# Kernel optimization log

Measured on AMD Instinct MI355X. Metric: run time of the kernel, lower is better.

The kernel has to match this reference:

```python
import jax, jax.numpy as jnp
import numpy as np

CHUNK_SIZE = 64
EPS = 1e-6


def setup_inputs() -> dict:
    key = jax.random.key(0)
    ks = jax.random.split(key, 5)
    B, NH, S, DH = 2, 16, 4096, 64
    return {
        "q": jax.random.normal(ks[0], (B, NH, S, DH), dtype=jnp.float32),
        "k": jax.random.normal(ks[1], (B, NH, S, DH), dtype=jnp.float32),
        "v": jax.random.normal(ks[2], (B, NH, S, DH), dtype=jnp.float32),
        "igate_preact": jax.random.normal(ks[3], (B, NH, S), dtype=jnp.float32),
        "fgate_preact": jax.random.normal(ks[4], (B, NH, S), dtype=jnp.float32),
    }


def _mlstm_intra(q, k, v, ig, fg, chunk_size, eps):
    # q,k,v: [B,NH,S,DH]; ig,fg: [B,NH,S]
    B, NH, S, DH = q.shape
    L = chunk_size
    NC = S // L
    qc = q.reshape(B, NH, NC, L, DH)
    kc = k.reshape(B, NH, NC, L, DH)
    vc = v.reshape(B, NH, NC, L, DH)
    igc = ig.reshape(B, NH, NC, L)
    fgc = fg.reshape(B, NH, NC, L)

    # log forget gates and their within-chunk cumulative sums
    log_fg = jax.nn.log_sigmoid(fgc)                      # [B,NH,NC,L]
    log_fg_cum = jnp.cumsum(log_fg, axis=-1)              # [B,NH,NC,L]

    # gated decay matrix: logD[i,j] = sum_{t=j+1..i} log f_t + i_j  for j<=i
    log_fg_mat = log_fg_cum[..., :, None] - log_fg_cum[..., None, :]  # [B,NH,NC,L,L]
    log_D = log_fg_mat + igc[..., None, :]
    causal = jnp.tril(jnp.ones((L, L), dtype=bool))
    log_D = jnp.where(causal, log_D, -jnp.inf)

    # stabilizer (row-wise max)
    m = jnp.max(log_D, axis=-1)                           # [B,NH,NC,L]
    D = jnp.exp(log_D - m[..., None])                     # [B,NH,NC,L,L]

    # QK scores scaled, gated by decay matrix
    scale = 1.0 / jnp.sqrt(jnp.asarray(DH, dtype=q.dtype))
    scores = jnp.einsum("bncld,bncsd->bncls", qc, kc) * scale
    C = scores * D                                        # [B,NH,NC,L,L]

    # stabilized normalizer: max(|row sum|, exp(-m))
    n = jnp.maximum(jnp.abs(jnp.sum(C, axis=-1)), jnp.exp(-m))  # [B,NH,NC,L]
    h = jnp.einsum("bncls,bncsd->bncld", C, vc) / (n[..., None] + eps)
    return h.reshape(B, NH, S, DH)


def reference(q, k, v, igate_preact, fgate_preact):
    return _mlstm_intra(q, k, v, igate_preact, fgate_preact, CHUNK_SIZE, EPS)
```

## Files before the change

kernel.cpp:

```cpp
#include <hip/hip_runtime.h>
#include <hip/hip_bf16.h>
#include <math.h>

namespace {

typedef __bf16 bf16x8 __attribute__((ext_vector_type(8)));
typedef float f32x4 __attribute__((ext_vector_type(4)));

constexpr int L = 64;
constexpr int DH = 64;

__device__ __forceinline__ int kkey(int r) { return (r ^ (r >> 2)) & 7; }
__device__ __forceinline__ int swzV(int d, int j) {
  return d * 128 + ((((j >> 3) ^ kkey(d)) & 7) << 4) + (j & 7) * 2;
}
__device__ __forceinline__ int swzC(int r, int j) {
  return r * 128 + ((((j >> 3) ^ kkey(r)) & 7) << 4) + (j & 7) * 2;
}

__device__ __forceinline__ unsigned short bfbits(float f) {
  __bf16 h = (__bf16)f;
  return __builtin_bit_cast(unsigned short, h);
}
__device__ __forceinline__ __bf16 tobf(float f) { return (__bf16)f; }

__global__ __launch_bounds__(64, 2) void mlstm_mfma(
    const float* __restrict__ q, const float* __restrict__ k,
    const float* __restrict__ v, const float* __restrict__ ig,
    const float* __restrict__ fg, float* __restrict__ out) {

  __shared__ __align__(16) char vt_raw[64 * 128];
  __shared__ __align__(16) char cs_raw[64 * 128];
  __shared__ __align__(16) float ea_sh[64];
  __shared__ float eb_sh[64], em_sh[64];

  const int lane = threadIdx.x;
  const int m = lane & 15;
  const int g = lane >> 4;
  const size_t cbase = (size_t)blockIdx.x * (L * DH);
  const size_t gb = (size_t)blockIdx.x * L;

  const float fgv = fg[gb + lane];
  const float igv = ig[gb + lane];

  const float4* v4 = (const float4*)(v + cbase);
  float4 vbuf[16];
#pragma unroll
  for (int it = 0; it < 16; ++it) vbuf[it] = v4[it * 64 + lane];

  float4 qbuf[4][2][2], kbuf[4][2][2];
#pragma unroll
  for (int rb = 0; rb < 4; ++rb)
#pragma unroll
    for (int kb = 0; kb < 2; ++kb) {
      const int off = (rb * 16 + m) * 64 + kb * 32 + g * 8;
      qbuf[rb][kb][0] = *(const float4*)(q + cbase + off);
      qbuf[rb][kb][1] = *(const float4*)(q + cbase + off + 4);
      kbuf[rb][kb][0] = *(const float4*)(k + cbase + off);
      kbuf[rb][kb][1] = *(const float4*)(k + cbase + off + 4);
    }

  {
    const float lf = fminf(fgv, 0.f) - log1pf(__expf(-fabsf(fgv)));
    float cum = lf;
#pragma unroll
    for (int o = 1; o < 64; o <<= 1) {
      const float t = __shfl_up(cum, o, 64);
      if (lane >= o) cum += t;
    }
    const float a = igv - cum;
    float b = a;
#pragma unroll
    for (int o = 1; o < 64; o <<= 1) {
      const float t = __shfl_up(b, o, 64);
      if (lane >= o) b = fmaxf(b, t);
    }
    const float bmax = __shfl(b, 63, 64);
    ea_sh[lane] = 0.125f * __expf(a - bmax);
    eb_sh[lane] = __expf(bmax - b);
    em_sh[lane] = __expf(-(b + cum));
  }

  {
    unsigned short* vt = (unsigned short*)vt_raw;
#pragma unroll
    for (int it = 0; it < 16; ++it) {
      const int idx = it * 64 + lane;
      const int j = idx >> 4;
      const int d0 = (idx & 15) * 4;
      vt[swzV(d0 + 0, j) >> 1] = bfbits(vbuf[it].x);
      vt[swzV(d0 + 1, j) >> 1] = bfbits(vbuf[it].y);
      vt[swzV(d0 + 2, j) >> 1] = bfbits(vbuf[it].z);
      vt[swzV(d0 + 3, j) >> 1] = bfbits(vbuf[it].w);
    }
  }

  bf16x8 qf[4][2], kf[4][2];
#pragma unroll
  for (int rb = 0; rb < 4; ++rb)
#pragma unroll
    for (int kb = 0; kb < 2; ++kb) {
      const float4 q0 = qbuf[rb][kb][0], q1 = qbuf[rb][kb][1];
      const float4 k0 = kbuf[rb][kb][0], k1 = kbuf[rb][kb][1];
      qf[rb][kb] = bf16x8{tobf(q0.x), tobf(q0.y), tobf(q0.z), tobf(q0.w),
                          tobf(q1.x), tobf(q1.y), tobf(q1.z), tobf(q1.w)};
      kf[rb][kb] = bf16x8{tobf(k0.x), tobf(k0.y), tobf(k0.z), tobf(k0.w),
                          tobf(k1.x), tobf(k1.y), tobf(k1.z), tobf(k1.w)};
    }

  f32x4 st[4][4];
#pragma unroll
  for (int cb = 0; cb < 4; ++cb)
#pragma unroll
    for (int rb = 0; rb < 4; ++rb) {
      if (rb > cb) continue;
      f32x4 acc = {0.f, 0.f, 0.f, 0.f};
      acc = __builtin_amdgcn_mfma_f32_16x16x32_bf16(kf[rb][0], qf[cb][0], acc, 0, 0, 0);
      acc = __builtin_amdgcn_mfma_f32_16x16x32_bf16(kf[rb][1], qf[cb][1], acc, 0, 0, 0);
      st[rb][cb] = acc;
    }

  bf16x8 vfr[4][2];
#pragma unroll
  for (int db = 0; db < 4; ++db)
#pragma unroll
    for (int jb = 0; jb < 2; ++jb)
      vfr[db][jb] =
          *(const bf16x8*)(vt_raw + swzV(db * 16 + m, jb * 32 + g * 8));

  float ea_j[4][4];
#pragma unroll
  for (int rb = 0; rb < 4; ++rb) {
    const float4 ea4 = *(const float4*)&ea_sh[rb * 16 + g * 4];
    ea_j[rb][0] = ea4.x; ea_j[rb][1] = ea4.y;
    ea_j[rb][2] = ea4.z; ea_j[rb][3] = ea4.w;
  }

  float invr[4];
#pragma unroll
  for (int cb = 0; cb < 4; ++cb) {
    const int i = cb * 16 + m;
    const float ebv = eb_sh[i];
    float rs = 0.f;
    const int rbfill = cb | 1;
#pragma unroll
    for (int rb = 0; rb < 4; ++rb) {
      if (rb > rbfill) continue;
      unsigned long long wp = 0ull;
      if (rb <= cb) {
#pragma unroll
        for (int e = 0; e < 4; ++e) {
          const int j = rb * 16 + g * 4 + e;
          const float val = (j <= i) ? st[rb][cb][e] * ea_j[rb][e] * ebv : 0.f;
          rs += val;
          wp |= (unsigned long long)bfbits(val) << (16 * e);
        }
      }
      *(unsigned long long*)(cs_raw + swzC(i, rb * 16 + g * 4)) = wp;
    }
    rs += __shfl_xor(rs, 16, 64);
    rs += __shfl_xor(rs, 32, 64);
    const float n = fmaxf(fabsf(rs), em_sh[i]);
    invr[cb] = 1.f / (n + 1e-6f);
  }

#pragma unroll
  for (int ib = 0; ib < 4; ++ib) {
    const int i = ib * 16 + m;
    const bf16x8 c0 = *(const bf16x8*)(cs_raw + swzC(i, g * 8));
    f32x4 acc[4];
#pragma unroll
    for (int db = 0; db < 4; ++db) {
      f32x4 z = {0.f, 0.f, 0.f, 0.f};
      acc[db] = __builtin_amdgcn_mfma_f32_16x16x32_bf16(vfr[db][0], c0, z, 0, 0, 0);
    }
    if (ib >= 2) {
      const bf16x8 c1 = *(const bf16x8*)(cs_raw + swzC(i, 32 + g * 8));
#pragma unroll
      for (int db = 0; db < 4; ++db)
        acc[db] = __builtin_amdgcn_mfma_f32_16x16x32_bf16(vfr[db][1], c1, acc[db], 0, 0, 0);
    }
    const float iv = invr[ib];
    float* op = out + cbase + i * 64 + g * 4;
#pragma unroll
    for (int db = 0; db < 4; ++db) {
      const f32x4 hv = acc[db];
      *(float4*)(op + db * 16) =
          make_float4(hv[0] * iv, hv[1] * iv, hv[2] * iv, hv[3] * iv);
    }
  }
}

}

extern "C" void kernel_launch(void* const* d_in, const int* in_sizes, int n_in,
                              void* d_out, int out_size, void* d_ws,
                              size_t ws_size, hipStream_t stream) {
  const float* q = (const float*)d_in[0];
  const float* k = (const float*)d_in[1];
  const float* v = (const float*)d_in[2];
  const float* ig = (const float*)d_in[3];
  const float* fg = (const float*)d_in[4];
  float* out = (float*)d_out;

  const int total = in_sizes[0];
  const int nchunks = total / (L * DH);
  mlstm_mfma<<<dim3(nchunks), dim3(64), 0, stream>>>(q, k, v, ig, fg, out);
}
```

Before: 27.68 us.

## Split each chunk across two wavefronts and pass gate factors via shuffles

```diff
diff --git a/kernel.cpp b/kernel.cpp
--- a/kernel.cpp
+++ b/kernel.cpp
@@ -24,17 +24,17 @@
 }
 __device__ __forceinline__ __bf16 tobf(float f) { return (__bf16)f; }
 
-__global__ __launch_bounds__(64, 2) void mlstm_mfma(
+__global__ __launch_bounds__(128, 4) void mlstm_mfma(
     const float* __restrict__ q, const float* __restrict__ k,
     const float* __restrict__ v, const float* __restrict__ ig,
     const float* __restrict__ fg, float* __restrict__ out) {
 
   __shared__ __align__(16) char vt_raw[64 * 128];
-  __shared__ __align__(16) char cs_raw[64 * 128];
-  __shared__ __align__(16) float ea_sh[64];
-  __shared__ float eb_sh[64], em_sh[64];
-
-  const int lane = threadIdx.x;
+  __shared__ __align__(16) char cs_raw[2][32 * 128];
+
+  const int tid = threadIdx.x;
+  const int w = tid >> 6;
+  const int lane = tid & 63;
   const int m = lane & 15;
   const int g = lane >> 4;
   const size_t cbase = (size_t)blockIdx.x * (L * DH);
@@ -44,22 +44,33 @@
   const float igv = ig[gb + lane];
 
   const float4* v4 = (const float4*)(v + cbase);
-  float4 vbuf[16];
-#pragma unroll
-  for (int it = 0; it < 16; ++it) vbuf[it] = v4[it * 64 + lane];
-
-  float4 qbuf[4][2][2], kbuf[4][2][2];
-#pragma unroll
-  for (int rb = 0; rb < 4; ++rb)
+  float4 vbuf[8];
+#pragma unroll
+  for (int it = 0; it < 8; ++it) vbuf[it] = v4[w * 512 + it * 64 + lane];
+
+  float4 qbuf[2][2][2];
+#pragma unroll
+  for (int lc = 0; lc < 2; ++lc)
 #pragma unroll
     for (int kb = 0; kb < 2; ++kb) {
-      const int off = (rb * 16 + m) * 64 + kb * 32 + g * 8;
-      qbuf[rb][kb][0] = *(const float4*)(q + cbase + off);
-      qbuf[rb][kb][1] = *(const float4*)(q + cbase + off + 4);
-      kbuf[rb][kb][0] = *(const float4*)(k + cbase + off);
-      kbuf[rb][kb][1] = *(const float4*)(k + cbase + off + 4);
-    }
-
+      const int off = ((2 * w + lc) * 16 + m) * 64 + kb * 32 + g * 8;
+      qbuf[lc][kb][0] = *(const float4*)(q + cbase + off);
+      qbuf[lc][kb][1] = *(const float4*)(q + cbase + off + 4);
+    }
+  float4 kbuf[4][2][2];
+#pragma unroll
+  for (int rb = 0; rb < 4; ++rb) {
+    if (rb <= 2 * w + 1) {
+#pragma unroll
+      for (int kb = 0; kb < 2; ++kb) {
+        const int off = (rb * 16 + m) * 64 + kb * 32 + g * 8;
+        kbuf[rb][kb][0] = *(const float4*)(k + cbase + off);
+        kbuf[rb][kb][1] = *(const float4*)(k + cbase + off + 4);
+      }
+    }
+  }
+
+  float ea, eb, em;
   {
     const float lf = fminf(fgv, 0.f) - log1pf(__expf(-fabsf(fgv)));
     float cum = lf;
@@ -76,16 +87,16 @@
       if (lane >= o) b = fmaxf(b, t);
     }
     const float bmax = __shfl(b, 63, 64);
-    ea_sh[lane] = 0.125f * __expf(a - bmax);
-    eb_sh[lane] = __expf(bmax - b);
-    em_sh[lane] = __expf(-(b + cum));
+    ea = 0.125f * __expf(a - bmax);
+    eb = __expf(bmax - b);
+    em = __expf(-(b + cum));
   }
 
   {
     unsigned short* vt = (unsigned short*)vt_raw;
 #pragma unroll
-    for (int it = 0; it < 16; ++it) {
-      const int idx = it * 64 + lane;
+    for (int it = 0; it < 8; ++it) {
+      const int idx = w * 512 + it * 64 + lane;
       const int j = idx >> 4;
       const int d0 = (idx & 15) * 4;
       vt[swzV(d0 + 0, j) >> 1] = bfbits(vbuf[it].x);
@@ -95,52 +106,68 @@
     }
   }
 
-  bf16x8 qf[4][2], kf[4][2];
+  bf16x8 qf[2][2], kf[4][2];
+#pragma unroll
+  for (int lc = 0; lc < 2; ++lc)
+#pragma unroll
+    for (int kb = 0; kb < 2; ++kb) {
+      const float4 q0 = qbuf[lc][kb][0], q1 = qbuf[lc][kb][1];
+      qf[lc][kb] = bf16x8{tobf(q0.x), tobf(q0.y), tobf(q0.z), tobf(q0.w),
+                          tobf(q1.x), tobf(q1.y), tobf(q1.z), tobf(q1.w)};
+    }
+#pragma unroll
+  for (int rb = 0; rb < 4; ++rb) {
+    if (rb <= 2 * w + 1) {
+#pragma unroll
+      for (int kb = 0; kb < 2; ++kb) {
+        const float4 k0 = kbuf[rb][kb][0], k1 = kbuf[rb][kb][1];
+        kf[rb][kb] = bf16x8{tobf(k0.x), tobf(k0.y), tobf(k0.z), tobf(k0.w),
+                            tobf(k1.x), tobf(k1.y), tobf(k1.z), tobf(k1.w)};
+      }
+    }
+  }
+
+  __syncthreads();
+
+  bf16x8 vfr[4][2];
+#pragma unroll
+  for (int db = 0; db < 4; ++db) {
+    vfr[db][0] = *(const bf16x8*)(vt_raw + swzV(db * 16 + m, g * 8));
+    if (w == 1)
+      vfr[db][1] = *(const bf16x8*)(vt_raw + swzV(db * 16 + m, 32 + g * 8));
+  }
+
+  f32x4 st[2][4];
+#pragma unroll
+  for (int lc = 0; lc < 2; ++lc) {
+    const int cb = 2 * w + lc;
+#pragma unroll
+    for (int rb = 0; rb < 4; ++rb) {
+      if (rb <= cb) {
+        f32x4 acc = {0.f, 0.f, 0.f, 0.f};
+        acc = __builtin_amdgcn_mfma_f32_16x16x32_bf16(kf[rb][0], qf[lc][0], acc, 0, 0, 0);
+        acc = __builtin_amdgcn_mfma_f32_16x16x32_bf16(kf[rb][1], qf[lc][1], acc, 0, 0, 0);
+        st[lc][rb] = acc;
+      }
+    }
+  }
+
+  float ea_j[4][4];
 #pragma unroll
   for (int rb = 0; rb < 4; ++rb)
 #pragma unroll
-    for (int kb = 0; kb < 2; ++kb) {
-      const float4 q0 = qbuf[rb][kb][0], q1 = qbuf[rb][kb][1];
-      const float4 k0 = kbuf[rb][kb][0], k1 = kbuf[rb][kb][1];
-      qf[rb][kb] = bf16x8{tobf(q0.x), tobf(q0.y), tobf(q0.z), tobf(q0.w),
-                          tobf(q1.x), tobf(q1.y), tobf(q1.z), tobf(q1.w)};
-      kf[rb][kb] = bf16x8{tobf(k0.x), tobf(k0.y), tobf(k0.z), tobf(k0.w),
-                          tobf(k1.x), tobf(k1.y), tobf(k1.z), tobf(k1.w)};
-    }
-
-  f32x4 st[4][4];
-#pragma unroll
-  for (int cb = 0; cb < 4; ++cb)
-#pragma unroll
-    for (int rb = 0; rb < 4; ++rb) {
-      if (rb > cb) continue;
-      f32x4 acc = {0.f, 0.f, 0.f, 0.f};
-      acc = __builtin_amdgcn_mfma_f32_16x16x32_bf16(kf[rb][0], qf[cb][0], acc, 0, 0, 0);
-      acc = __builtin_amdgcn_mfma_f32_16x16x32_bf16(kf[rb][1], qf[cb][1], acc, 0, 0, 0);
-      st[rb][cb] = acc;
-    }
-
-  bf16x8 vfr[4][2];
-#pragma unroll
-  for (int db = 0; db < 4; ++db)
-#pragma unroll
-    for (int jb = 0; jb < 2; ++jb)
-      vfr[db][jb] =
-          *(const bf16x8*)(vt_raw + swzV(db * 16 + m, jb * 32 + g * 8));
-
-  float ea_j[4][4];
-#pragma unroll
-  for (int rb = 0; rb < 4; ++rb) {
-    const float4 ea4 = *(const float4*)&ea_sh[rb * 16 + g * 4];
-    ea_j[rb][0] = ea4.x; ea_j[rb][1] = ea4.y;
-    ea_j[rb][2] = ea4.z; ea_j[rb][3] = ea4.w;
-  }
-
-  float invr[4];
-#pragma unroll
-  for (int cb = 0; cb < 4; ++cb) {
+    for (int e = 0; e < 4; ++e)
+      ea_j[rb][e] = __shfl(ea, rb * 16 + g * 4 + e, 64);
+
+  char* cw = cs_raw[w];
+  float invr[2];
+#pragma unroll
+  for (int lc = 0; lc < 2; ++lc) {
+    const int cb = 2 * w + lc;
     const int i = cb * 16 + m;
-    const float ebv = eb_sh[i];
+    const int r = lc * 16 + m;
+    const float ebv = __shfl(eb, i, 64);
+    const float emv = __shfl(em, i, 64);
     float rs = 0.f;
     const int rbfill = cb | 1;
 #pragma unroll
@@ -151,36 +178,36 @@
 #pragma unroll
         for (int e = 0; e < 4; ++e) {
           const int j = rb * 16 + g * 4 + e;
-          const float val = (j <= i) ? st[rb][cb][e] * ea_j[rb][e] * ebv : 0.f;
+          const float val = (j <= i) ? st[lc][rb][e] * ea_j[rb][e] * ebv : 0.f;
           rs += val;
           wp |= (unsigned long long)bfbits(val) << (16 * e);
         }
       }
-      *(unsigned long long*)(cs_raw + swzC(i, rb * 16 + g * 4)) = wp;
+      *(unsigned long long*)(cw + swzC(r, rb * 16 + g * 4)) = wp;
     }
     rs += __shfl_xor(rs, 16, 64);
     rs += __shfl_xor(rs, 32, 64);
-    const float n = fmaxf(fabsf(rs), em_sh[i]);
-    invr[cb] = 1.f / (n + 1e-6f);
-  }
-
-#pragma unroll
-  for (int ib = 0; ib < 4; ++ib) {
-    const int i = ib * 16 + m;
-    const bf16x8 c0 = *(const bf16x8*)(cs_raw + swzC(i, g * 8));
+    invr[lc] = 1.f / (fmaxf(fabsf(rs), emv) + 1e-6f);
+  }
+
+#pragma unroll
+  for (int lc = 0; lc < 2; ++lc) {
+    const int i = (2 * w + lc) * 16 + m;
+    const int r = lc * 16 + m;
+    const bf16x8 c0 = *(const bf16x8*)(cw + swzC(r, g * 8));
     f32x4 acc[4];
 #pragma unroll
     for (int db = 0; db < 4; ++db) {
       f32x4 z = {0.f, 0.f, 0.f, 0.f};
       acc[db] = __builtin_amdgcn_mfma_f32_16x16x32_bf16(vfr[db][0], c0, z, 0, 0, 0);
     }
-    if (ib >= 2) {
-      const bf16x8 c1 = *(const bf16x8*)(cs_raw + swzC(i, 32 + g * 8));
+    if (w == 1) {
+      const bf16x8 c1 = *(const bf16x8*)(cw + swzC(r, 32 + g * 8));
 #pragma unroll
       for (int db = 0; db < 4; ++db)
         acc[db] = __builtin_amdgcn_mfma_f32_16x16x32_bf16(vfr[db][1], c1, acc[db], 0, 0, 0);
     }
-    const float iv = invr[ib];
+    const float iv = invr[lc];
     float* op = out + cbase + i * 64 + g * 4;
 #pragma unroll
     for (int db = 0; db < 4; ++db) {
@@ -205,5 +232,5 @@
 
   const int total = in_sizes[0];
   const int nchunks = total / (L * DH);
-  mlstm_mfma<<<dim3(nchunks), dim3(64), 0, stream>>>(q, k, v, ig, fg, out);
-}
+  mlstm_mfma<<<dim3(nchunks), dim3(128), 0, stream>>>(q, k, v, ig, fg, out);
+}
```

Result: slower. 31.66 us (+14.4%).
